# Kernel tuning notes

Hardware: AMD Instinct MI355X
Metric: run time of the kernel (lower is better)

The kernel has to match this reference:

```python
import jax, jax.numpy as jnp
import numpy as np

B, D, E, K = 8192, 1024, 8, 5  # batch, in_dim, num_size_classes, num_depth_classes
H = max(64, D)                 # hidden = max(64, in_dim)
EPS = 1e-8


def ordinal_logits_to_probs(logits, num_classes):
    # logits: [B, K-1] cumulative ordinal logits -> [B, K] class probs
    q = jax.nn.sigmoid(logits)
    probs = jnp.concatenate(
        [1.0 - q[:, :1], q[:, :-1] - q[:, 1:], q[:, -1:]], axis=1
    )  # [B, K]
    probs = jnp.clip(probs, EPS)
    return probs / jnp.clip(probs.sum(axis=1, keepdims=True), EPS)


def setup_inputs() -> dict:
    key = jax.random.key(0)
    kx, ks, k1, k2 = jax.random.split(key, 4)
    x = jax.random.normal(kx, (B, D), dtype=jnp.float32)
    size_idx = jax.random.randint(ks, (B,), 0, E, dtype=jnp.int64)
    # per-expert 2-layer MLP params: Linear(D,H) -> ReLU -> Linear(H,K-1)
    W1 = jax.random.normal(k1, (E, D, H), dtype=jnp.float32) / np.sqrt(D)
    b1 = jnp.zeros((E, H), dtype=jnp.float32)
    W2 = jax.random.normal(k2, (E, H, K - 1), dtype=jnp.float32) / np.sqrt(H)
    b2 = jnp.zeros((E, K - 1), dtype=jnp.float32)
    return {"x": x, "size_idx": size_idx, "W1": W1, "b1": b1, "W2": W2, "b2": b2}


def reference(x, size_idx, W1, b1, W2, b2):
    # Hard routing: each token gets the output of expert size_idx[b].
    # Dense all-expert compute + per-token select (same math as mask/gather/scatter,
    # dropout is inference-mode identity).
    h = jax.nn.relu(jnp.einsum('bd,edh->beh', x, W1) + b1)      # [B, E, H]
    all_logits = jnp.einsum('beh,ehk->bek', h, W2) + b2          # [B, E, K-1]
    idx = size_idx.astype(jnp.int32)[:, None, None]              # [B, 1, 1]
    logits = jnp.take_along_axis(all_logits, idx, axis=1)[:, 0]  # [B, K-1]
    probs = ordinal_logits_to_probs(logits, K)                   # [B, K]
    return logits, probs
```

## Files before the change

kernel.cpp:

```cpp
#include <hip/hip_runtime.h>
#include <cstdint>
#include <cstddef>

#define Bn 8192
#define Dn 1024
#define Hn 1024
#define En 8
#define MT 128
#define NTILE 64
#define NB (Hn / NTILE)
#define MAX_TILES (Bn / MT + En)
#define PERM_N (Bn + En * MT)

typedef unsigned short u16;
typedef __bf16 bf16x8 __attribute__((ext_vector_type(8)));
typedef float f32x4 __attribute__((ext_vector_type(4)));
typedef unsigned short ushort8 __attribute__((ext_vector_type(8)));

__device__ __forceinline__ u16 f2bf(float f) {
  unsigned int u = __float_as_uint(f);
  unsigned int r = u + 0x7fffu + ((u >> 16) & 1u);
  return (u16)(r >> 16);
}

__device__ __forceinline__ void gld16(const void* g, void* l) {
  __builtin_amdgcn_global_load_lds(
      (const __attribute__((address_space(1))) void*)g,
      (__attribute__((address_space(3))) void*)l, 16, 0, 0);
}

__global__ __launch_bounds__(1024) void route_k(const int* __restrict__ sidx,
                                                int* __restrict__ off,
                                                int* __restrict__ perm) {
  __shared__ int hist[16][En];
  __shared__ int base[16][En];
  __shared__ int eoff[En + 1];
  int t = threadIdx.x;
  int wv = t >> 6;
  if (t < 16 * En) ((int*)hist)[t] = 0;
  __syncthreads();
  int e8[8], r8[8];
#pragma unroll
  for (int i = 0; i < 8; i++) {
    int e = sidx[t + i * 1024];
    e8[i] = e;
    r8[i] = atomicAdd(&hist[wv][e], 1);
  }
  __syncthreads();
  if (t < En) {
    int s = 0;
    for (int w = 0; w < 16; w++) { base[w][t] = s; s += hist[w][t]; }
    hist[0][t] = s;
  }
  __syncthreads();
  if (t == 0) {
    int o = 0;
    for (int e = 0; e < En; e++) {
      eoff[e] = o; off[e] = o;
      o += (hist[0][e] + MT - 1) & ~(MT - 1);
    }
    eoff[En] = o; off[En] = o;
  }
  __syncthreads();
#pragma unroll
  for (int i = 0; i < 8; i++) {
    int e = e8[i];
    perm[eoff[e] + base[wv][e] + r8[i]] = t + i * 1024;
  }
}

__global__ __launch_bounds__(256) void cvt_xp_k(const float* __restrict__ x,
                                                const int* __restrict__ perm,
                                                u16* __restrict__ xbp) {
  size_t idx = ((size_t)blockIdx.x * 256 + threadIdx.x) * 8;
  int p = (int)(idx >> 10);
  int col = (int)(idx & 1023);
  int tok = perm[p];
  ushort8 o;
  if (tok < 0) {
    o = (ushort8){0, 0, 0, 0, 0, 0, 0, 0};
  } else {
    const float* src = x + ((size_t)tok << 10) + col;
    float4 a = *(const float4*)src;
    float4 b = *(const float4*)(src + 4);
    o[0] = f2bf(a.x); o[1] = f2bf(a.y); o[2] = f2bf(a.z); o[3] = f2bf(a.w);
    o[4] = f2bf(b.x); o[5] = f2bf(b.y); o[6] = f2bf(b.z); o[7] = f2bf(b.w);
  }
  *(ushort8*)(xbp + idx) = o;
}

__global__ __launch_bounds__(256) void cvt_w1_k(const float* __restrict__ W1,
                                                u16* __restrict__ W1t) {
  __shared__ float tile[64][65];
  int e = blockIdx.z;
  int k0 = blockIdx.y * 64;
  int n0 = blockIdx.x * 64;
  int c4 = (threadIdx.x & 15) * 4;
  int r0 = threadIdx.x >> 4;
  const float* src = W1 + ((size_t)e << 20) + (size_t)k0 * Hn + n0;
#pragma unroll
  for (int i = 0; i < 4; i++) {
    int r = r0 + i * 16;
    float4 v = *(const float4*)(src + (size_t)r * Hn + c4);
    tile[r][c4 + 0] = v.x; tile[r][c4 + 1] = v.y;
    tile[r][c4 + 2] = v.z; tile[r][c4 + 3] = v.w;
  }
  __syncthreads();
  u16* dst = W1t + ((size_t)e << 20) + (size_t)n0 * Dn + k0;
#pragma unroll
  for (int i = 0; i < 4; i++) {
    int h = r0 + i * 16;
    ushort4 o;
    o.x = f2bf(tile[c4 + 0][h]);
    o.y = f2bf(tile[c4 + 1][h]);
    o.z = f2bf(tile[c4 + 2][h]);
    o.w = f2bf(tile[c4 + 3][h]);
    *(ushort4*)(dst + (size_t)h * Dn + c4) = o;
  }
}

__global__ __launch_bounds__(256) void gemm_k(
    const u16* __restrict__ xbp, const u16* __restrict__ w1t,
    const float* __restrict__ b1, const float* __restrict__ w2,
    const int* __restrict__ off, float* __restrict__ partials) {
  __shared__ u16 As[2][128 * 32];
  __shared__ u16 Bs[2][64 * 32];

  int tb = blockIdx.x;
  int row0 = tb * MT;
  if (row0 >= off[En]) return;
  int e = 0;
  while (row0 >= off[e + 1]) e++;
  int n0 = blockIdx.y * NTILE;

  int tid = threadIdx.x;
  int lane = tid & 63, w = tid >> 6;

  int srow = lane >> 2;
  int slot = lane & 3;
  int scol = (slot ^ ((srow >> 1) & 3)) * 8;
  const u16* aG[2]; u16* aL[2];
#pragma unroll
  for (int j = 0; j < 2; j++) {
    int rl = 32 * w + 16 * j + srow;
    aG[j] = xbp + (size_t)(row0 + rl) * Dn + scol;
    aL[j] = (u16*)As + (32 * w + 16 * j) * 32;
  }
  const u16* bG = w1t + ((size_t)e << 20) + (size_t)(n0 + 16 * w + srow) * Dn + scol;
  u16* bL = (u16*)Bs + (16 * w) * 32;

  f32x4 acc[2][4];
#pragma unroll
  for (int i = 0; i < 2; i++)
#pragma unroll
    for (int j = 0; j < 4; j++)
      acc[i][j] = (f32x4){0.f, 0.f, 0.f, 0.f};

  int fr = lane & 15;
  int qf = lane >> 4;
  int qs = (qf ^ ((fr >> 1) & 3)) * 8;
  int offA[2], offB[4];
#pragma unroll
  for (int i = 0; i < 2; i++) offA[i] = (w * 32 + i * 16 + fr) * 32 + qs;
#pragma unroll
  for (int j = 0; j < 4; j++) offB[j] = (j * 16 + fr) * 32 + qs;

  gld16(aG[0], aL[0]); gld16(aG[1], aL[1]); gld16(bG, bL);

  int cur = 0;
  for (int k0 = 0; k0 < Dn; k0 += 32, cur ^= 1) {
    __syncthreads();
    if (k0 + 32 < Dn) {
      int nb = cur ^ 1;
      gld16(aG[0] + k0 + 32, aL[0] + nb * 4096);
      gld16(aG[1] + k0 + 32, aL[1] + nb * 4096);
      gld16(bG + k0 + 32, bL + nb * 2048);
    }
    const u16* Ab = (const u16*)As + cur * 4096;
    const u16* Bb = (const u16*)Bs + cur * 2048;
    bf16x8 af[2], bfr[4];
#pragma unroll
    for (int i = 0; i < 2; i++) af[i] = *(const bf16x8*)(Ab + offA[i]);
#pragma unroll
    for (int j = 0; j < 4; j++) bfr[j] = *(const bf16x8*)(Bb + offB[j]);
#pragma unroll
    for (int i = 0; i < 2; i++)
#pragma unroll
      for (int j = 0; j < 4; j++)
        acc[i][j] = __builtin_amdgcn_mfma_f32_16x16x32_bf16(af[i], bfr[j], acc[i][j], 0, 0, 0);
  }

  float4 w2v[4]; float b1v[4];
#pragma unroll
  for (int j = 0; j < 4; j++) {
    int col = n0 + j * 16 + fr;
    w2v[j] = *(const float4*)(w2 + ((size_t)e * Hn + col) * 4);
    b1v[j] = b1[(size_t)e * Hn + col];
  }
#pragma unroll
  for (int i = 0; i < 2; i++) {
#pragma unroll
    for (int r = 0; r < 4; r++) {
      float s0 = 0.f, s1 = 0.f, s2 = 0.f, s3 = 0.f;
#pragma unroll
      for (int j = 0; j < 4; j++) {
        float h = acc[i][j][r] + b1v[j];
        h = fmaxf(h, 0.f);
        s0 = fmaf(h, w2v[j].x, s0);
        s1 = fmaf(h, w2v[j].y, s1);
        s2 = fmaf(h, w2v[j].z, s2);
        s3 = fmaf(h, w2v[j].w, s3);
      }
#pragma unroll
      for (int m = 1; m < 16; m <<= 1) {
        s0 += __shfl_xor(s0, m);
        s1 += __shfl_xor(s1, m);
        s2 += __shfl_xor(s2, m);
        s3 += __shfl_xor(s3, m);
      }
      if (fr == 0) {
        int row = w * 32 + i * 16 + qf * 4 + r;
        *(float4*)(partials + ((size_t)(row0 + row) * NB + blockIdx.y) * 4) =
            make_float4(s0, s1, s2, s3);
      }
    }
  }
}

__global__ void probs_k(const float* __restrict__ partials,
                        const int* __restrict__ perm, const int* __restrict__ off,
                        const int* __restrict__ sidx, const float* __restrict__ b2,
                        float* __restrict__ out) {
  int p = blockIdx.x * blockDim.x + threadIdx.x;
  if (p >= off[En]) return;
  int tok = perm[p];
  if (tok < 0) return;
  int e = sidx[tok];
  float s0 = 0.f, s1 = 0.f, s2 = 0.f, s3 = 0.f;
#pragma unroll
  for (int nb = 0; nb < NB; nb++) {
    float4 v = *(const float4*)(partials + ((size_t)p * NB + nb) * 4);
    s0 += v.x; s1 += v.y; s2 += v.z; s3 += v.w;
  }
  float l0 = s0 + b2[e * 4 + 0];
  float l1 = s1 + b2[e * 4 + 1];
  float l2 = s2 + b2[e * 4 + 2];
  float l3 = s3 + b2[e * 4 + 3];
  out[tok * 4 + 0] = l0; out[tok * 4 + 1] = l1;
  out[tok * 4 + 2] = l2; out[tok * 4 + 3] = l3;
  float q0 = 1.f / (1.f + expf(-l0));
  float q1 = 1.f / (1.f + expf(-l1));
  float q2 = 1.f / (1.f + expf(-l2));
  float q3 = 1.f / (1.f + expf(-l3));
  const float eps = 1e-8f;
  float p0 = fmaxf(1.f - q0, eps);
  float p1 = fmaxf(q0 - q1, eps);
  float p2 = fmaxf(q1 - q2, eps);
  float p3 = fmaxf(q2 - q3, eps);
  float p4 = fmaxf(q3, eps);
  float s = p0 + p1 + p2 + p3 + p4;
  float inv = 1.f / fmaxf(s, eps);
  float* pr = out + (size_t)Bn * 4 + (size_t)tok * 5;
  pr[0] = p0 * inv; pr[1] = p1 * inv; pr[2] = p2 * inv;
  pr[3] = p3 * inv; pr[4] = p4 * inv;
}

extern "C" void kernel_launch(void* const* d_in, const int* in_sizes, int n_in,
                              void* d_out, int out_size, void* d_ws, size_t ws_size,
                              hipStream_t stream) {
  const float* x  = (const float*)d_in[0];
  const int* sidx = (const int*)d_in[1];
  const float* W1 = (const float*)d_in[2];
  const float* b1 = (const float*)d_in[3];
  const float* W2 = (const float*)d_in[4];
  const float* b2 = (const float*)d_in[5];
  float* out = (float*)d_out;

  uint8_t* w = (uint8_t*)d_ws;
  int* off  = (int*)(w + 64);
  int* perm = (int*)(w + 512);
  u16* xbp      = (u16*)(w + 40960);
  u16* w1t      = (u16*)(w + 18919424);
  float* parts  = (float*)(w + 35700736);

  hipMemsetAsync(perm, 0xFF, PERM_N * sizeof(int), stream);

  route_k<<<1, 1024, 0, stream>>>(sidx, off, perm);
  cvt_xp_k<<<(PERM_N * Dn) / (256 * 8), 256, 0, stream>>>(x, perm, xbp);
  cvt_w1_k<<<dim3(Hn / 64, Dn / 64, En), 256, 0, stream>>>(W1, w1t);
  gemm_k<<<dim3(MAX_TILES, NB), 256, 0, stream>>>(xbp, w1t, b1, W2, off, parts);
  probs_k<<<(PERM_N + 255) / 256, 256, 0, stream>>>(parts, perm, off, sidx, b2, out);
}
```

Measured before the change: 174.7 us.

## Enlarge GEMM tile to 128x128 with triple-buffered LDS pipeline and fold memset

Widens the grouped GEMM block tile from 128x64 to 128x128 with a 2x2 wave layout, so each wave computes a 64x64 sub-tile with 16 MFMAs per k-step. The k-loop is fully unrolled into a three-stage LDS ring with explicit vmcnt waits, keeping two loads in flight. The grid is reordered so N-tiles are the fast dimension, which should improve L2 reuse of x rows. The perm memset is moved into route_k to drop a separate launch. In exchange, the kernel uses more LDS and accumulator registers, which may reduce occupancy.

```diff
diff --git a/kernel.cpp b/kernel.cpp
--- a/kernel.cpp
+++ b/kernel.cpp
@@ -7,9 +7,8 @@
 #define Hn 1024
 #define En 8
 #define MT 128
-#define NTILE 64
-#define NB (Hn / NTILE)
-#define MAX_TILES (Bn / MT + En)
+#define NB 16
+#define MTILES (Bn / MT + En)
 #define PERM_N (Bn + En * MT)
 
 typedef unsigned short u16;
@@ -28,6 +27,19 @@
       (const __attribute__((address_space(1))) void*)g,
       (__attribute__((address_space(3))) void*)l, 16, 0, 0);
 }
+
+#define PIPE_BARRIER_VM4() do {                    \
+    asm volatile("" ::: "memory");                 \
+    __builtin_amdgcn_s_waitcnt(0x0F74);            \
+    __builtin_amdgcn_s_barrier();                  \
+    asm volatile("" ::: "memory");                 \
+  } while (0)
+#define PIPE_BARRIER_VM0() do {                    \
+    asm volatile("" ::: "memory");                 \
+    __builtin_amdgcn_s_waitcnt(0x0F70);            \
+    __builtin_amdgcn_s_barrier();                  \
+    asm volatile("" ::: "memory");                 \
+  } while (0)
 
 __global__ __launch_bounds__(1024) void route_k(const int* __restrict__ sidx,
                                                 int* __restrict__ off,
@@ -38,6 +50,8 @@
   int t = threadIdx.x;
   int wv = t >> 6;
   if (t < 16 * En) ((int*)hist)[t] = 0;
+#pragma unroll
+  for (int i = 0; i < PERM_N / 1024; i++) perm[t + i * 1024] = -1;
   __syncthreads();
   int e8[8], r8[8];
 #pragma unroll
@@ -123,35 +137,35 @@
     const u16* __restrict__ xbp, const u16* __restrict__ w1t,
     const float* __restrict__ b1, const float* __restrict__ w2,
     const int* __restrict__ off, float* __restrict__ partials) {
-  __shared__ u16 As[2][128 * 32];
-  __shared__ u16 Bs[2][64 * 32];
-
-  int tb = blockIdx.x;
-  int row0 = tb * MT;
+  __shared__ u16 As[3][4096];
+  __shared__ u16 Bs[3][4096];
+
+  int n0 = blockIdx.x * 128;
+  int row0 = blockIdx.y * MT;
   if (row0 >= off[En]) return;
   int e = 0;
   while (row0 >= off[e + 1]) e++;
-  int n0 = blockIdx.y * NTILE;
 
   int tid = threadIdx.x;
   int lane = tid & 63, w = tid >> 6;
+  int wm = w >> 1, wn = w & 1;
 
   int srow = lane >> 2;
   int slot = lane & 3;
   int scol = (slot ^ ((srow >> 1) & 3)) * 8;
-  const u16* aG[2]; u16* aL[2];
+  const u16* aG[2]; const u16* bG[2];
+  int lOff[2];
 #pragma unroll
   for (int j = 0; j < 2; j++) {
     int rl = 32 * w + 16 * j + srow;
     aG[j] = xbp + (size_t)(row0 + rl) * Dn + scol;
-    aL[j] = (u16*)As + (32 * w + 16 * j) * 32;
-  }
-  const u16* bG = w1t + ((size_t)e << 20) + (size_t)(n0 + 16 * w + srow) * Dn + scol;
-  u16* bL = (u16*)Bs + (16 * w) * 32;
-
-  f32x4 acc[2][4];
-#pragma unroll
-  for (int i = 0; i < 2; i++)
+    bG[j] = w1t + ((size_t)e << 20) + (size_t)(n0 + rl) * Dn + scol;
+    lOff[j] = (32 * w + 16 * j) * 32;
+  }
+
+  f32x4 acc[4][4];
+#pragma unroll
+  for (int i = 0; i < 4; i++)
 #pragma unroll
     for (int j = 0; j < 4; j++)
       acc[i][j] = (f32x4){0.f, 0.f, 0.f, 0.f};
@@ -159,46 +173,75 @@
   int fr = lane & 15;
   int qf = lane >> 4;
   int qs = (qf ^ ((fr >> 1) & 3)) * 8;
-  int offA[2], offB[4];
-#pragma unroll
-  for (int i = 0; i < 2; i++) offA[i] = (w * 32 + i * 16 + fr) * 32 + qs;
-#pragma unroll
-  for (int j = 0; j < 4; j++) offB[j] = (j * 16 + fr) * 32 + qs;
-
-  gld16(aG[0], aL[0]); gld16(aG[1], aL[1]); gld16(bG, bL);
-
-  int cur = 0;
-  for (int k0 = 0; k0 < Dn; k0 += 32, cur ^= 1) {
-    __syncthreads();
-    if (k0 + 32 < Dn) {
-      int nb = cur ^ 1;
-      gld16(aG[0] + k0 + 32, aL[0] + nb * 4096);
-      gld16(aG[1] + k0 + 32, aL[1] + nb * 4096);
-      gld16(bG + k0 + 32, bL + nb * 2048);
+  int offA[4], offB[4];
+#pragma unroll
+  for (int i = 0; i < 4; i++)
+    offA[i] = (wm * 64 + i * 16 + fr) * 32 + qs;
+#pragma unroll
+  for (int j = 0; j < 4; j++)
+    offB[j] = (wn * 64 + j * 16 + fr) * 32 + qs;
+
+#pragma unroll
+  for (int it = 0; it < 2; it++) {
+    int ko = it * 32;
+    gld16(aG[0] + ko, (u16*)As[it] + lOff[0]);
+    gld16(aG[1] + ko, (u16*)As[it] + lOff[1]);
+    gld16(bG[0] + ko, (u16*)Bs[it] + lOff[0]);
+    gld16(bG[1] + ko, (u16*)Bs[it] + lOff[1]);
+  }
+
+#pragma unroll
+  for (int i = 0; i < 31; i++) {
+    PIPE_BARRIER_VM4();
+    if (i + 2 < 32) {
+      int s = (i + 2) % 3;
+      int ko = (i + 2) * 32;
+      gld16(aG[0] + ko, (u16*)As[s] + lOff[0]);
+      gld16(aG[1] + ko, (u16*)As[s] + lOff[1]);
+      gld16(bG[0] + ko, (u16*)Bs[s] + lOff[0]);
+      gld16(bG[1] + ko, (u16*)Bs[s] + lOff[1]);
     }
-    const u16* Ab = (const u16*)As + cur * 4096;
-    const u16* Bb = (const u16*)Bs + cur * 2048;
-    bf16x8 af[2], bfr[4];
-#pragma unroll
-    for (int i = 0; i < 2; i++) af[i] = *(const bf16x8*)(Ab + offA[i]);
-#pragma unroll
-    for (int j = 0; j < 4; j++) bfr[j] = *(const bf16x8*)(Bb + offB[j]);
-#pragma unroll
-    for (int i = 0; i < 2; i++)
-#pragma unroll
-      for (int j = 0; j < 4; j++)
-        acc[i][j] = __builtin_amdgcn_mfma_f32_16x16x32_bf16(af[i], bfr[j], acc[i][j], 0, 0, 0);
-  }
-
+    const u16* Ab = (const u16*)As[i % 3];
+    const u16* Bb = (const u16*)Bs[i % 3];
+    bf16x8 af[4], bfr[4];
+#pragma unroll
+    for (int ii = 0; ii < 4; ii++) af[ii] = *(const bf16x8*)(Ab + offA[ii]);
+#pragma unroll
+    for (int jj = 0; jj < 4; jj++) bfr[jj] = *(const bf16x8*)(Bb + offB[jj]);
+#pragma unroll
+    for (int ii = 0; ii < 4; ii++)
+#pragma unroll
+      for (int jj = 0; jj < 4; jj++)
+        acc[ii][jj] = __builtin_amdgcn_mfma_f32_16x16x32_bf16(af[ii], bfr[jj], acc[ii][jj], 0, 0, 0);
+  }
+  {
+    PIPE_BARRIER_VM0();
+    const u16* Ab = (const u16*)As[31 % 3];
+    const u16* Bb = (const u16*)Bs[31 % 3];
+    bf16x8 af[4], bfr[4];
+#pragma unroll
+    for (int ii = 0; ii < 4; ii++) af[ii] = *(const bf16x8*)(Ab + offA[ii]);
+#pragma unroll
+    for (int jj = 0; jj < 4; jj++) bfr[jj] = *(const bf16x8*)(Bb + offB[jj]);
+#pragma unroll
+    for (int ii = 0; ii < 4; ii++)
+#pragma unroll
+      for (int jj = 0; jj < 4; jj++)
+        acc[ii][jj] = __builtin_amdgcn_mfma_f32_16x16x32_bf16(af[ii], bfr[jj], acc[ii][jj], 0, 0, 0);
+  }
+
+  int fq = lane >> 4;
   float4 w2v[4]; float b1v[4];
 #pragma unroll
   for (int j = 0; j < 4; j++) {
-    int col = n0 + j * 16 + fr;
+    int col = n0 + wn * 64 + j * 16 + fr;
     w2v[j] = *(const float4*)(w2 + ((size_t)e * Hn + col) * 4);
     b1v[j] = b1[(size_t)e * Hn + col];
   }
-#pragma unroll
-  for (int i = 0; i < 2; i++) {
+  int chunk = blockIdx.x * 2 + wn;
+#pragma unroll
+  for (int i = 0; i < 4; i++) {
+    int rbase = wm * 64 + i * 16 + fq * 4;
 #pragma unroll
     for (int r = 0; r < 4; r++) {
       float s0 = 0.f, s1 = 0.f, s2 = 0.f, s3 = 0.f;
@@ -219,8 +262,8 @@
         s3 += __shfl_xor(s3, m);
       }
       if (fr == 0) {
-        int row = w * 32 + i * 16 + qf * 4 + r;
-        *(float4*)(partials + ((size_t)(row0 + row) * NB + blockIdx.y) * 4) =
+        int row = row0 + rbase + r;
+        *(float4*)(partials + ((size_t)row * NB + chunk) * 4) =
             make_float4(s0, s1, s2, s3);
       }
     }
@@ -283,11 +326,9 @@
   u16* w1t      = (u16*)(w + 18919424);
   float* parts  = (float*)(w + 35700736);
 
-  hipMemsetAsync(perm, 0xFF, PERM_N * sizeof(int), stream);
-
   route_k<<<1, 1024, 0, stream>>>(sidx, off, perm);
   cvt_xp_k<<<(PERM_N * Dn) / (256 * 8), 256, 0, stream>>>(x, perm, xbp);
   cvt_w1_k<<<dim3(Hn / 64, Dn / 64, En), 256, 0, stream>>>(W1, w1t);
-  gemm_k<<<dim3(MAX_TILES, NB), 256, 0, stream>>>(xbp, w1t, b1, W2, off, parts);
+  gemm_k<<<dim3(Hn / 128, MTILES), 256, 0, stream>>>(xbp, w1t, b1, W2, off, parts);
   probs_k<<<(PERM_N + 255) / 256, 256, 0, stream>>>(parts, perm, off, sidx, b2, out);
 }
```

Result: faster. 160.6 us (-8.1%).

## Retile expert GEMM to 64x128 with 2x2 waves and fuse prep kernels

Applied to the files above, without the earlier changes.

The GEMM block tile changes from 128 rows x 64 hidden to 64 rows x 128 hidden, with a 2x2 wave layout. The grid now puts the hidden-chunk index in blockIdx.x, so blocks that share a row tile launch next to each other, and consecutive row tiles usually belong to the same expert. The x and W1 bf16 conversion kernels are merged into one launch, and the perm memset moves into route_k, which removes two launches. In exchange, the smaller M tile loads each W1 tile for more row tiles, which raises total global and L2 traffic for the weight operand.

```diff
diff --git a/kernel.cpp b/kernel.cpp
--- a/kernel.cpp
+++ b/kernel.cpp
@@ -7,10 +7,12 @@
 #define Hn 1024
 #define En 8
 #define MT 128
-#define NTILE 64
-#define NB (Hn / NTILE)
-#define MAX_TILES (Bn / MT + En)
+#define MTILE 64
+#define NB 16
+#define MTILES (PERM_N / MTILE)
 #define PERM_N (Bn + En * MT)
+#define XBLKS ((PERM_N * Dn) / (256 * 8))
+#define WBLKS (16 * 16 * En)
 
 typedef unsigned short u16;
 typedef __bf16 bf16x8 __attribute__((ext_vector_type(8)));
@@ -38,6 +40,8 @@
   int t = threadIdx.x;
   int wv = t >> 6;
   if (t < 16 * En) ((int*)hist)[t] = 0;
+#pragma unroll
+  for (int i = 0; i < PERM_N / 1024; i++) perm[t + i * 1024] = -1;
   __syncthreads();
   int e8[8], r8[8];
 #pragma unroll
@@ -69,53 +73,56 @@
   }
 }
 
-__global__ __launch_bounds__(256) void cvt_xp_k(const float* __restrict__ x,
-                                                const int* __restrict__ perm,
-                                                u16* __restrict__ xbp) {
-  size_t idx = ((size_t)blockIdx.x * 256 + threadIdx.x) * 8;
-  int p = (int)(idx >> 10);
-  int col = (int)(idx & 1023);
-  int tok = perm[p];
-  ushort8 o;
-  if (tok < 0) {
-    o = (ushort8){0, 0, 0, 0, 0, 0, 0, 0};
+__global__ __launch_bounds__(256) void cvt_k(const float* __restrict__ x,
+                                             const int* __restrict__ perm,
+                                             u16* __restrict__ xbp,
+                                             const float* __restrict__ W1,
+                                             u16* __restrict__ W1t) {
+  __shared__ float tile[64][65];
+  int bid = blockIdx.x;
+  if (bid < XBLKS) {
+    size_t idx = ((size_t)bid * 256 + threadIdx.x) * 8;
+    int p = (int)(idx >> 10);
+    int col = (int)(idx & 1023);
+    int tok = perm[p];
+    ushort8 o;
+    if (tok < 0) {
+      o = (ushort8){0, 0, 0, 0, 0, 0, 0, 0};
+    } else {
+      const float* src = x + ((size_t)tok << 10) + col;
+      float4 a = *(const float4*)src;
+      float4 b = *(const float4*)(src + 4);
+      o[0] = f2bf(a.x); o[1] = f2bf(a.y); o[2] = f2bf(a.z); o[3] = f2bf(a.w);
+      o[4] = f2bf(b.x); o[5] = f2bf(b.y); o[6] = f2bf(b.z); o[7] = f2bf(b.w);
+    }
+    *(ushort8*)(xbp + idx) = o;
   } else {
-    const float* src = x + ((size_t)tok << 10) + col;
-    float4 a = *(const float4*)src;
-    float4 b = *(const float4*)(src + 4);
-    o[0] = f2bf(a.x); o[1] = f2bf(a.y); o[2] = f2bf(a.z); o[3] = f2bf(a.w);
-    o[4] = f2bf(b.x); o[5] = f2bf(b.y); o[6] = f2bf(b.z); o[7] = f2bf(b.w);
-  }
-  *(ushort8*)(xbp + idx) = o;
-}
-
-__global__ __launch_bounds__(256) void cvt_w1_k(const float* __restrict__ W1,
-                                                u16* __restrict__ W1t) {
-  __shared__ float tile[64][65];
-  int e = blockIdx.z;
-  int k0 = blockIdx.y * 64;
-  int n0 = blockIdx.x * 64;
-  int c4 = (threadIdx.x & 15) * 4;
-  int r0 = threadIdx.x >> 4;
-  const float* src = W1 + ((size_t)e << 20) + (size_t)k0 * Hn + n0;
-#pragma unroll
-  for (int i = 0; i < 4; i++) {
-    int r = r0 + i * 16;
-    float4 v = *(const float4*)(src + (size_t)r * Hn + c4);
-    tile[r][c4 + 0] = v.x; tile[r][c4 + 1] = v.y;
-    tile[r][c4 + 2] = v.z; tile[r][c4 + 3] = v.w;
-  }
-  __syncthreads();
-  u16* dst = W1t + ((size_t)e << 20) + (size_t)n0 * Dn + k0;
-#pragma unroll
-  for (int i = 0; i < 4; i++) {
-    int h = r0 + i * 16;
-    ushort4 o;
-    o.x = f2bf(tile[c4 + 0][h]);
-    o.y = f2bf(tile[c4 + 1][h]);
-    o.z = f2bf(tile[c4 + 2][h]);
-    o.w = f2bf(tile[c4 + 3][h]);
-    *(ushort4*)(dst + (size_t)h * Dn + c4) = o;
+    int wb = bid - XBLKS;
+    int e = wb >> 8;
+    int k0 = ((wb >> 4) & 15) * 64;
+    int n0 = (wb & 15) * 64;
+    int c4 = (threadIdx.x & 15) * 4;
+    int r0 = threadIdx.x >> 4;
+    const float* src = W1 + ((size_t)e << 20) + (size_t)k0 * Hn + n0;
+#pragma unroll
+    for (int i = 0; i < 4; i++) {
+      int r = r0 + i * 16;
+      float4 v = *(const float4*)(src + (size_t)r * Hn + c4);
+      tile[r][c4 + 0] = v.x; tile[r][c4 + 1] = v.y;
+      tile[r][c4 + 2] = v.z; tile[r][c4 + 3] = v.w;
+    }
+    __syncthreads();
+    u16* dst = W1t + ((size_t)e << 20) + (size_t)n0 * Dn + k0;
+#pragma unroll
+    for (int i = 0; i < 4; i++) {
+      int h = r0 + i * 16;
+      ushort4 o;
+      o.x = f2bf(tile[c4 + 0][h]);
+      o.y = f2bf(tile[c4 + 1][h]);
+      o.z = f2bf(tile[c4 + 2][h]);
+      o.w = f2bf(tile[c4 + 3][h]);
+      *(ushort4*)(dst + (size_t)h * Dn + c4) = o;
+    }
   }
 }
 
@@ -123,31 +130,32 @@
     const u16* __restrict__ xbp, const u16* __restrict__ w1t,
     const float* __restrict__ b1, const float* __restrict__ w2,
     const int* __restrict__ off, float* __restrict__ partials) {
-  __shared__ u16 As[2][128 * 32];
-  __shared__ u16 Bs[2][64 * 32];
-
-  int tb = blockIdx.x;
-  int row0 = tb * MT;
+  __shared__ u16 As[2][MTILE * 32];
+  __shared__ u16 Bs[2][128 * 32];
+
+  int n0 = blockIdx.x * 128;
+  int row0 = blockIdx.y * MTILE;
   if (row0 >= off[En]) return;
   int e = 0;
   while (row0 >= off[e + 1]) e++;
-  int n0 = blockIdx.y * NTILE;
 
   int tid = threadIdx.x;
   int lane = tid & 63, w = tid >> 6;
+  int wm = w >> 1, wn = w & 1;
 
   int srow = lane >> 2;
   int slot = lane & 3;
   int scol = (slot ^ ((srow >> 1) & 3)) * 8;
-  const u16* aG[2]; u16* aL[2];
+  const u16* aG = xbp + (size_t)(row0 + 16 * w + srow) * Dn + scol;
+  int lOffA = (16 * w) * 32;
+  const u16* bG[2];
+  int lOffB[2];
 #pragma unroll
   for (int j = 0; j < 2; j++) {
     int rl = 32 * w + 16 * j + srow;
-    aG[j] = xbp + (size_t)(row0 + rl) * Dn + scol;
-    aL[j] = (u16*)As + (32 * w + 16 * j) * 32;
-  }
-  const u16* bG = w1t + ((size_t)e << 20) + (size_t)(n0 + 16 * w + srow) * Dn + scol;
-  u16* bL = (u16*)Bs + (16 * w) * 32;
+    bG[j] = w1t + ((size_t)e << 20) + (size_t)(n0 + rl) * Dn + scol;
+    lOffB[j] = (32 * w + 16 * j) * 32;
+  }
 
   f32x4 acc[2][4];
 #pragma unroll
@@ -161,23 +169,25 @@
   int qs = (qf ^ ((fr >> 1) & 3)) * 8;
   int offA[2], offB[4];
 #pragma unroll
-  for (int i = 0; i < 2; i++) offA[i] = (w * 32 + i * 16 + fr) * 32 + qs;
-#pragma unroll
-  for (int j = 0; j < 4; j++) offB[j] = (j * 16 + fr) * 32 + qs;
-
-  gld16(aG[0], aL[0]); gld16(aG[1], aL[1]); gld16(bG, bL);
+  for (int i = 0; i < 2; i++) offA[i] = (wm * 32 + i * 16 + fr) * 32 + qs;
+#pragma unroll
+  for (int j = 0; j < 4; j++) offB[j] = (wn * 64 + j * 16 + fr) * 32 + qs;
+
+  gld16(aG, (u16*)As[0] + lOffA);
+  gld16(bG[0], (u16*)Bs[0] + lOffB[0]);
+  gld16(bG[1], (u16*)Bs[0] + lOffB[1]);
 
   int cur = 0;
   for (int k0 = 0; k0 < Dn; k0 += 32, cur ^= 1) {
     __syncthreads();
     if (k0 + 32 < Dn) {
       int nb = cur ^ 1;
-      gld16(aG[0] + k0 + 32, aL[0] + nb * 4096);
-      gld16(aG[1] + k0 + 32, aL[1] + nb * 4096);
-      gld16(bG + k0 + 32, bL + nb * 2048);
-    }
-    const u16* Ab = (const u16*)As + cur * 4096;
-    const u16* Bb = (const u16*)Bs + cur * 2048;
+      gld16(aG + k0 + 32, (u16*)As[nb] + lOffA);
+      gld16(bG[0] + k0 + 32, (u16*)Bs[nb] + lOffB[0]);
+      gld16(bG[1] + k0 + 32, (u16*)Bs[nb] + lOffB[1]);
+    }
+    const u16* Ab = (const u16*)As[cur];
+    const u16* Bb = (const u16*)Bs[cur];
     bf16x8 af[2], bfr[4];
 #pragma unroll
     for (int i = 0; i < 2; i++) af[i] = *(const bf16x8*)(Ab + offA[i]);
@@ -190,15 +200,18 @@
         acc[i][j] = __builtin_amdgcn_mfma_f32_16x16x32_bf16(af[i], bfr[j], acc[i][j], 0, 0, 0);
   }
 
+  int fq = lane >> 4;
   float4 w2v[4]; float b1v[4];
 #pragma unroll
   for (int j = 0; j < 4; j++) {
-    int col = n0 + j * 16 + fr;
+    int col = n0 + wn * 64 + j * 16 + fr;
     w2v[j] = *(const float4*)(w2 + ((size_t)e * Hn + col) * 4);
     b1v[j] = b1[(size_t)e * Hn + col];
   }
+  int chunk = blockIdx.x * 2 + wn;
 #pragma unroll
   for (int i = 0; i < 2; i++) {
+    int rbase = wm * 32 + i * 16 + fq * 4;
 #pragma unroll
     for (int r = 0; r < 4; r++) {
       float s0 = 0.f, s1 = 0.f, s2 = 0.f, s3 = 0.f;
@@ -219,8 +232,8 @@
         s3 += __shfl_xor(s3, m);
       }
       if (fr == 0) {
-        int row = w * 32 + i * 16 + qf * 4 + r;
-        *(float4*)(partials + ((size_t)(row0 + row) * NB + blockIdx.y) * 4) =
+        int row = row0 + rbase + r;
+        *(float4*)(partials + ((size_t)row * NB + chunk) * 4) =
             make_float4(s0, s1, s2, s3);
       }
     }
@@ -283,11 +296,8 @@
   u16* w1t      = (u16*)(w + 18919424);
   float* parts  = (float*)(w + 35700736);
 
-  hipMemsetAsync(perm, 0xFF, PERM_N * sizeof(int), stream);
-
   route_k<<<1, 1024, 0, stream>>>(sidx, off, perm);
-  cvt_xp_k<<<(PERM_N * Dn) / (256 * 8), 256, 0, stream>>>(x, perm, xbp);
-  cvt_w1_k<<<dim3(Hn / 64, Dn / 64, En), 256, 0, stream>>>(W1, w1t);
-  gemm_k<<<dim3(MAX_TILES, NB), 256, 0, stream>>>(xbp, w1t, b1, W2, off, parts);
+  cvt_k<<<XBLKS + WBLKS, 256, 0, stream>>>(x, perm, xbp, W1, w1t);
+  gemm_k<<<dim3(Hn / 128, MTILES), 256, 0, stream>>>(xbp, w1t, b1, W2, off, parts);
   probs_k<<<(PERM_N + 255) / 256, 256, 0, stream>>>(parts, perm, off, sidx, b2, out);
 }
```

New measurement: 170.8 us. 1.02x faster.
